# Kernel tuning notes

Hardware: AMD Instinct MI355X
Metric: run time of the kernel (lower is better)

Reference implementation:

```python
import jax, jax.numpy as jnp
import numpy as np

B, SQ, SKV, D = 16, 2048, 2048, 256

def setup_inputs() -> dict:
    key = jax.random.key(0)
    k1, k2, k3 = jax.random.split(key, 3)
    x = jax.random.normal(k1, (B, SQ, D), dtype=jnp.float32)
    y = jax.random.normal(k2, (B, SKV, D), dtype=jnp.float32)
    attn_mask = jax.random.normal(k3, (B, SQ, SKV), dtype=jnp.float32)
    dropout = 0  # p=0 -> deterministic (F.dropout with p=0 is identity)
    return {"x": x, "y": y, "attn_mask": attn_mask, "dropout": dropout}

def reference(x, y, attn_mask, dropout):
    # qk = x @ y^T : [B, Sq, Skv]
    qk = jnp.einsum('bqd,bkd->bqk', x, y)
    # NOTE: original scales mask by 1/sqrt(y.size(-2)) = 1/sqrt(Skv), not sqrt(D)
    scale_factor = attn_mask / (y.shape[-2] ** 0.5)
    scaled_qk = qk * scale_factor  # multiplicative per-element mask
    softmax_qk = jax.nn.softmax(scaled_qk, axis=-1)
    # dropout p=0 -> identity (deterministic baseline)
    dropout_qk = softmax_qk
    output = jnp.einsum('bqk,bkd->bqd', dropout_qk, y)
    return output + x
```

## Files before the change

kernel.cpp:

```cpp
#include <hip/hip_runtime.h>
#include <stdint.h>

typedef unsigned short u16;
typedef unsigned int   u32;

#define NB   16
#define SQL  2048
#define SKVL 2048
#define DHD  256
#define SCALE 0.022097086912079612f

typedef __bf16 bf16x8 __attribute__((ext_vector_type(8)));
typedef float  f32x4  __attribute__((ext_vector_type(4)));
typedef float  f32x16 __attribute__((ext_vector_type(16)));

__device__ __forceinline__ u16 f2b(float f) {
    union { float f; u32 i; } v; v.f = f;
    u32 x = v.i;
    return (u16)((x + 0x7fffu + ((x >> 16) & 1u)) >> 16);
}

__device__ __forceinline__ void async_cp16(const void* g, void* l) {
    __builtin_amdgcn_global_load_lds(
        (const __attribute__((address_space(1))) u32*)g,
        (__attribute__((address_space(3))) u32*)l, 16, 0, 0);
}

__global__ __launch_bounds__(256)
void prepass(const float* __restrict__ y, u16* __restrict__ ws)
{
    u16* yb  = ws;
    u16* ybT = ws + 8388608;

    const int tid = threadIdx.x;
    if (blockIdx.x < 512) {
        const int b   = blockIdx.x >> 5;
        const int seg = blockIdx.x & 31;
        const int r   = tid >> 2;
        const int dq  = tid & 3;
        const int kvg = seg * 64 + r;
        const float* src = y + ((size_t)(b * SKVL + kvg)) * DHD + dq * 64;
        u16* dst = yb + ((size_t)(b * SKVL + kvg)) * DHD;
        #pragma unroll
        for (int j = 0; j < 8; ++j) {
            const float4 a = *(const float4*)(src + j * 8);
            const float4 c4 = *(const float4*)(src + j * 8 + 4);
            union { u32 w[4]; uint4 q; } u;
            u.w[0] = (u32)f2b(a.x)  | ((u32)f2b(a.y)  << 16);
            u.w[1] = (u32)f2b(a.z)  | ((u32)f2b(a.w)  << 16);
            u.w[2] = (u32)f2b(c4.x) | ((u32)f2b(c4.y) << 16);
            u.w[3] = (u32)f2b(c4.z) | ((u32)f2b(c4.w) << 16);
            const int pos = (dq * 8 + j) ^ (kvg & 7);
            *(uint4*)(dst + pos * 8) = u.q;
        }
    } else {
        const int j     = blockIdx.x - 512;
        const int b     = j >> 5;
        const int kvblk = j & 31;
        const int d     = tid;
        const int kv0   = kvblk * 64;
        u16* dst = ybT + ((size_t)(b * 32 + kvblk)) * 16384 + d * 64;
        #pragma unroll
        for (int c = 0; c < 8; ++c) {
            float v[8];
            #pragma unroll
            for (int e = 0; e < 8; ++e)
                v[e] = y[((size_t)(b * SKVL + kv0 + 8 * c + e)) * DHD + d];
            union { u32 w[4]; uint4 q; } u;
            #pragma unroll
            for (int i = 0; i < 4; ++i)
                u.w[i] = (u32)f2b(v[2 * i]) | ((u32)f2b(v[2 * i + 1]) << 16);
            const int p = c ^ (d & 7);
            *(uint4*)(dst + p * 8) = u.q;
        }
    }
}

#define WAITBAR(str)                                          \
    do {                                                      \
        asm volatile("s_waitcnt " str ::: "memory");          \
        __builtin_amdgcn_sched_barrier(0);                    \
        __builtin_amdgcn_s_barrier();                         \
        __builtin_amdgcn_sched_barrier(0);                    \
    } while (0)

__global__ __launch_bounds__(256, 2)
void fa_main(const float* __restrict__ x, const float* __restrict__ mask,
             const u16* __restrict__ ws, float* __restrict__ out)
{
    __shared__ __align__(16) u16 Ks[16384];
    __shared__ __align__(16) u16 Vt[16384];
    __shared__ __align__(16) u16 Ps[64 * 72];
    __shared__ float Lred[2][64];

    const u16* yb  = ws;
    const u16* ybT = ws + 8388608;

    const int tid  = threadIdx.x;
    const int wv   = tid >> 6;
    const int lane = tid & 63;
    const int n    = lane & 31;
    const int hi   = lane >> 5;
    const int qh   = wv & 1;
    const int kh   = wv >> 1;

    const int b  = blockIdx.x >> 5;
    const int q0 = (blockIdx.x & 31) * 64;

    bf16x8 qfrag[16];
    {
        const float* xq = x + ((size_t)(b * SQL + q0 + 32 * qh + n)) * DHD + 8 * hi;
        #pragma unroll
        for (int s = 0; s < 16; ++s) {
            const float4 a  = *(const float4*)(xq + s * 16);
            const float4 c4 = *(const float4*)(xq + s * 16 + 4);
            union { u32 w[4]; bf16x8 v; } u;
            u.w[0] = (u32)f2b(a.x)  | ((u32)f2b(a.y)  << 16);
            u.w[1] = (u32)f2b(a.z)  | ((u32)f2b(a.w)  << 16);
            u.w[2] = (u32)f2b(c4.x) | ((u32)f2b(c4.y) << 16);
            u.w[3] = (u32)f2b(c4.z) | ((u32)f2b(c4.w) << 16);
            qfrag[s] = u.v;
        }
    }

    f32x16 o0 = {}, o1 = {}, o2 = {}, o3 = {};
    float lsum[16];
    #pragma unroll
    for (int r = 0; r < 16; ++r) lsum[r] = 0.f;

    const float* mrow = mask + ((size_t)(b * SQL + q0 + 32 * qh + 4 * hi)) * SKVL
                             + 32 * kh + n;
    #define ROFF(r) ((size_t)(((r) & 3) + 8 * ((r) >> 2)) * SKVL)

    float mkc[16], mkn[16];
    #pragma unroll
    for (int r = 0; r < 16; ++r) mkc[r] = mrow[ROFF(r)];

    {
        const char* gk = (const char*)(yb + ((size_t)b * SKVL) * DHD) + wv * 8192 + lane * 16;
        const char* gv = (const char*)(ybT + ((size_t)b * 32) * 16384) + wv * 8192 + lane * 16;
        char* lk = ((char*)Ks) + wv * 8192;
        char* lv = ((char*)Vt) + wv * 8192;
        #pragma unroll
        for (int i = 0; i < 8; ++i) { async_cp16(gk + i * 1024, lk + i * 1024);
                                      async_cp16(gv + i * 1024, lv + i * 1024); }
    }
    WAITBAR("vmcnt(0) lgkmcnt(0)");

    for (int it = 0; it < 32; ++it) {
        const size_t kvn = (it + 1 < 32) ? (size_t)(it + 1) * 64 : 0;
        #pragma unroll
        for (int r = 0; r < 16; ++r) mkn[r] = mrow[ROFF(r) + kvn];

        f32x16 sacc = {};
        const int kvloc = 32 * kh + n;
        __builtin_amdgcn_s_setprio(1);
        #pragma unroll
        for (int s = 0; s < 16; ++s) {
            const int p = (2 * s + hi) ^ (kvloc & 7);
            bf16x8 bf = *(const bf16x8*)(&Ks[kvloc * 256 + p * 8]);
            sacc = __builtin_amdgcn_mfma_f32_32x32x16_bf16(qfrag[s], bf, sacc, 0, 0, 0);
        }
        __builtin_amdgcn_s_setprio(0);

        #pragma unroll
        for (int r = 0; r < 16; ++r) {
            const int rowloc = (r & 3) + 8 * (r >> 2) + 4 * hi;
            float pv = __expf(sacc[r] * mkc[r] * SCALE);
            lsum[r] += pv;
            Ps[(32 * qh + rowloc) * 72 + 32 * kh + n] = f2b(pv);
        }

        WAITBAR("vmcnt(16) lgkmcnt(0)");

        if (it + 1 < 32) {
            const char* gk = (const char*)(yb + ((size_t)(b * SKVL + (it + 1) * 64)) * DHD)
                             + wv * 8192 + lane * 16;
            char* lk = ((char*)Ks) + wv * 8192;
            #pragma unroll
            for (int i = 0; i < 8; ++i) async_cp16(gk + i * 1024, lk + i * 1024);
        }

        bf16x8 pa[4];
        #pragma unroll
        for (int s = 0; s < 4; ++s)
            pa[s] = *(const bf16x8*)(&Ps[(32 * qh + n) * 72 + 16 * s + 8 * hi]);
        __builtin_amdgcn_s_setprio(1);
        #pragma unroll
        for (int t = 0; t < 4; ++t) {
            const int d = 128 * kh + 32 * t + n;
            f32x16 acc = (t == 0) ? o0 : (t == 1) ? o1 : (t == 2) ? o2 : o3;
            #pragma unroll
            for (int s = 0; s < 4; ++s) {
                const int p = (2 * s + hi) ^ (d & 7);
                bf16x8 bf = *(const bf16x8*)(&Vt[d * 64 + p * 8]);
                acc = __builtin_amdgcn_mfma_f32_32x32x16_bf16(pa[s], bf, acc, 0, 0, 0);
            }
            if (t == 0) o0 = acc; else if (t == 1) o1 = acc; else if (t == 2) o2 = acc; else o3 = acc;
        }
        __builtin_amdgcn_s_setprio(0);

        WAITBAR("lgkmcnt(0)");

        if (it + 1 < 32) {
            const char* gv = (const char*)(ybT + ((size_t)(b * 32 + it + 1)) * 16384)
                             + wv * 8192 + lane * 16;
            char* lv = ((char*)Vt) + wv * 8192;
            #pragma unroll
            for (int i = 0; i < 8; ++i) async_cp16(gv + i * 1024, lv + i * 1024);
        }

        WAITBAR("vmcnt(8) lgkmcnt(0)");

        #pragma unroll
        for (int r = 0; r < 16; ++r) mkc[r] = mkn[r];
    }

    #pragma unroll
    for (int r = 0; r < 16; ++r) {
        float v = lsum[r];
        v += __shfl_xor(v, 1);
        v += __shfl_xor(v, 2);
        v += __shfl_xor(v, 4);
        v += __shfl_xor(v, 8);
        v += __shfl_xor(v, 16);
        if (n == 0) {
            const int rowloc = (r & 3) + 8 * (r >> 2) + 4 * hi;
            Lred[kh][32 * qh + rowloc] = v;
        }
    }
    __syncthreads();

    float inv[16];
    #pragma unroll
    for (int r = 0; r < 16; ++r) {
        const int qloc = 32 * qh + (r & 3) + 8 * (r >> 2) + 4 * hi;
        inv[r] = 1.0f / (Lred[0][qloc] + Lred[1][qloc]);
    }

    #pragma unroll
    for (int r = 0; r < 16; ++r) {
        const int qloc = 32 * qh + (r & 3) + 8 * (r >> 2) + 4 * hi;
        const size_t rowoff = ((size_t)(b * SQL + q0 + qloc)) * DHD;
        #pragma unroll
        for (int t = 0; t < 4; ++t) {
            const int d = 128 * kh + 32 * t + n;
            const float ov = (t == 0) ? o0[r] : (t == 1) ? o1[r] : (t == 2) ? o2[r] : o3[r];
            out[rowoff + d] = ov * inv[r] + x[rowoff + d];
        }
    }
}

#define FKSS 264
#define FVTG 328
#define FPSS 40

__global__ __launch_bounds__(256, 2)
void fa_fallback(const float* __restrict__ x, const float* __restrict__ y,
                 const float* __restrict__ mask, float* __restrict__ out)
{
    __shared__ __align__(16) u16 Ks[32 * FKSS];
    __shared__ __align__(16) u32 Vt[16 * FVTG];
    __shared__ __align__(16) u16 Ps[64 * FPSS];

    const int tid  = threadIdx.x;
    const int wv   = tid >> 6;
    const int lane = tid & 63;
    const int l16  = lane & 15;
    const int quad = lane >> 4;
    const int b  = blockIdx.x >> 5;
    const int q0 = (blockIdx.x & 31) * 64;

    bf16x8 qfrag[8];
    {
        const float* xq = x + ((size_t)(b * SQL + q0 + wv * 16 + l16)) * DHD + quad * 8;
        #pragma unroll
        for (int s = 0; s < 8; ++s) {
            const float4 a = *(const float4*)(xq + s * 32);
            const float4 c = *(const float4*)(xq + s * 32 + 4);
            union { u32 w[4]; bf16x8 v; } u;
            u.w[0] = (u32)f2b(a.x) | ((u32)f2b(a.y) << 16);
            u.w[1] = (u32)f2b(a.z) | ((u32)f2b(a.w) << 16);
            u.w[2] = (u32)f2b(c.x) | ((u32)f2b(c.y) << 16);
            u.w[3] = (u32)f2b(c.z) | ((u32)f2b(c.w) << 16);
            qfrag[s] = u.v;
        }
    }
    f32x4 o[16] = {};
    float ls[4] = {0.f, 0.f, 0.f, 0.f};
    const int kv2 = tid & 15;
    const int dc  = tid >> 4;
    const float* ybase = y + ((size_t)b * SKVL) * DHD;
    float4 r0[4], r1[4];
    {
        const float* p0 = ybase + (size_t)(2 * kv2) * DHD + dc * 16;
        const float* p1 = p0 + DHD;
        #pragma unroll
        for (int p = 0; p < 4; ++p) { r0[p] = *(const float4*)(p0 + p * 4);
                                      r1[p] = *(const float4*)(p1 + p * 4); }
    }
    const float* mbase = mask + ((size_t)(b * SQL + q0 + wv * 16 + quad * 4)) * SKVL;
    float mkc0[4], mkc1[4], mkn0[4], mkn1[4];
    #pragma unroll
    for (int r = 0; r < 4; ++r) {
        const float* mp = mbase + (size_t)r * SKVL;
        mkc0[r] = mp[l16]; mkc1[r] = mp[16 + l16];
    }
    for (int it = 0; it < 64; ++it) {
        const int kv0 = it * 32;
        __syncthreads();
        {
            u16 e0[16], e1[16];
            #pragma unroll
            for (int p = 0; p < 4; ++p) {
                e0[p*4+0]=f2b(r0[p].x); e0[p*4+1]=f2b(r0[p].y);
                e0[p*4+2]=f2b(r0[p].z); e0[p*4+3]=f2b(r0[p].w);
                e1[p*4+0]=f2b(r1[p].x); e1[p*4+1]=f2b(r1[p].y);
                e1[p*4+2]=f2b(r1[p].z); e1[p*4+3]=f2b(r1[p].w);
            }
            union { u32 w[4]; uint4 q; } k0a, k0b, k1a, k1b;
            #pragma unroll
            for (int i = 0; i < 4; ++i) {
                k0a.w[i] = (u32)e0[2*i]   | ((u32)e0[2*i+1]   << 16);
                k0b.w[i] = (u32)e0[8+2*i] | ((u32)e0[8+2*i+1] << 16);
                k1a.w[i] = (u32)e1[2*i]   | ((u32)e1[2*i+1]   << 16);
                k1b.w[i] = (u32)e1[8+2*i] | ((u32)e1[8+2*i+1] << 16);
            }
            *(uint4*)(&Ks[(2*kv2)  *FKSS + dc*16])     = k0a.q;
            *(uint4*)(&Ks[(2*kv2)  *FKSS + dc*16 + 8]) = k0b.q;
            *(uint4*)(&Ks[(2*kv2+1)*FKSS + dc*16])     = k1a.q;
            *(uint4*)(&Ks[(2*kv2+1)*FKSS + dc*16 + 8]) = k1b.q;
            #pragma unroll
            for (int e = 0; e < 16; ++e)
                Vt[dc*FVTG + e*20 + kv2] = (u32)e0[e] | ((u32)e1[e] << 16);
        }
        __syncthreads();
        if (it + 1 < 64) {
            const float* p0 = ybase + (size_t)(kv0 + 32 + 2 * kv2) * DHD + dc * 16;
            const float* p1 = p0 + DHD;
            #pragma unroll
            for (int p = 0; p < 4; ++p) { r0[p] = *(const float4*)(p0 + p * 4);
                                          r1[p] = *(const float4*)(p1 + p * 4); }
        }
        {
            const int kvn2 = (it + 1 < 64) ? (kv0 + 32) : 0;
            #pragma unroll
            for (int r = 0; r < 4; ++r) {
                const float* mp = mbase + (size_t)r * SKVL + kvn2;
                mkn0[r] = mp[l16]; mkn1[r] = mp[16 + l16];
            }
        }
        f32x4 acc0 = {}, acc1 = {};
        #pragma unroll
        for (int s = 0; s < 8; ++s) {
            bf16x8 b0 = *(const bf16x8*)(&Ks[ l16     * FKSS + s*32 + quad*8]);
            bf16x8 b1 = *(const bf16x8*)(&Ks[(16+l16) * FKSS + s*32 + quad*8]);
            acc0 = __builtin_amdgcn_mfma_f32_16x16x32_bf16(qfrag[s], b0, acc0, 0, 0, 0);
            acc1 = __builtin_amdgcn_mfma_f32_16x16x32_bf16(qfrag[s], b1, acc1, 0, 0, 0);
        }
        #pragma unroll
        for (int r = 0; r < 4; ++r) {
            float p0 = __expf(acc0[r] * mkc0[r] * SCALE);
            float p1 = __expf(acc1[r] * mkc1[r] * SCALE);
            ls[r] += p0 + p1;
            u16* pr = &Ps[(wv*16 + quad*4 + r) * FPSS];
            pr[l16]      = f2b(p0);
            pr[16 + l16] = f2b(p1);
        }
        bf16x8 afrag = *(const bf16x8*)(&Ps[(wv*16 + l16) * FPSS + quad*8]);
        #pragma unroll
        for (int t = 0; t < 16; ++t) {
            bf16x8 bfrag = *(const bf16x8*)(&Vt[t*FVTG + l16*20 + quad*4]);
            o[t] = __builtin_amdgcn_mfma_f32_16x16x32_bf16(afrag, bfrag, o[t], 0, 0, 0);
        }
        #pragma unroll
        for (int r = 0; r < 4; ++r) { mkc0[r] = mkn0[r]; mkc1[r] = mkn1[r]; }
    }
    #pragma unroll
    for (int r = 0; r < 4; ++r) {
        float v = ls[r];
        v += __shfl_xor(v, 1); v += __shfl_xor(v, 2);
        v += __shfl_xor(v, 4); v += __shfl_xor(v, 8);
        ls[r] = 1.0f / v;
    }
    const int qrow = q0 + wv * 16 + quad * 4;
    #pragma unroll
    for (int r = 0; r < 4; ++r) {
        const size_t rowoff = ((size_t)(b * SQL + qrow + r)) * DHD;
        #pragma unroll
        for (int t = 0; t < 16; ++t) {
            const int d = t * 16 + l16;
            out[rowoff + d] = o[t][r] * ls[r] + x[rowoff + d];
        }
    }
}

extern "C" void kernel_launch(void* const* d_in, const int* in_sizes, int n_in,
                              void* d_out, int out_size, void* d_ws, size_t ws_size,
                              hipStream_t stream) {
    const float* x    = (const float*)d_in[0];
    const float* y    = (const float*)d_in[1];
    const float* mask = (const float*)d_in[2];
    float* out        = (float*)d_out;

    if (ws_size >= 33554432ull) {
        prepass<<<1024, 256, 0, stream>>>(y, (u16*)d_ws);
        fa_main<<<512, 256, 0, stream>>>(x, mask, (const u16*)d_ws, out);
    } else {
        fa_fallback<<<512, 256, 0, stream>>>(x, y, mask, out);
    }
}
```

Before: 469.8 us.

## Load V fragments directly from global in MFMA layout and double-buffer K in LDS

The prepass now writes V in a per-lane MFMA fragment layout, so each wave loads its V operand straight from global memory into registers and never stages it through LDS. The LDS space freed by dropping the V buffer becomes a second K buffer, giving K double-buffering with a single barrier pair per iteration instead of three. The K swizzle widens from 8 to 32 slots, and the mask prefetch moves to after the softmax. In exchange, each iteration now waits for all outstanding memory loads at its end, and the V register arrays raise register pressure.

```diff
diff --git a/kernel.cpp b/kernel.cpp
--- a/kernel.cpp
+++ b/kernel.cpp
@@ -30,7 +30,7 @@
 void prepass(const float* __restrict__ y, u16* __restrict__ ws)
 {
     u16* yb  = ws;
-    u16* ybT = ws + 8388608;
+    u16* ybF = ws + 8388608;
 
     const int tid = threadIdx.x;
     if (blockIdx.x < 512) {
@@ -50,18 +50,21 @@
             u.w[1] = (u32)f2b(a.z)  | ((u32)f2b(a.w)  << 16);
             u.w[2] = (u32)f2b(c4.x) | ((u32)f2b(c4.y) << 16);
             u.w[3] = (u32)f2b(c4.z) | ((u32)f2b(c4.w) << 16);
-            const int pos = (dq * 8 + j) ^ (kvg & 7);
+            const int pos = (dq * 8 + j) ^ (kvg & 31);
             *(uint4*)(dst + pos * 8) = u.q;
         }
     } else {
         const int j     = blockIdx.x - 512;
         const int b     = j >> 5;
-        const int kvblk = j & 31;
+        const int it    = j & 31;
         const int d     = tid;
-        const int kv0   = kvblk * 64;
-        u16* dst = ybT + ((size_t)(b * 32 + kvblk)) * 16384 + d * 64;
+        const int kv0   = it * 64;
+        const int kh = d >> 7, t = (d >> 5) & 3, n = d & 31;
+        u16* dst = ybF + ((size_t)(b * 32 + it)) * 16384 + kh * 8192 + t * 2048 + n * 8;
         #pragma unroll
         for (int c = 0; c < 8; ++c) {
+            const int s  = c >> 1;
+            const int hi = c & 1;
             float v[8];
             #pragma unroll
             for (int e = 0; e < 8; ++e)
@@ -70,8 +73,7 @@
             #pragma unroll
             for (int i = 0; i < 4; ++i)
                 u.w[i] = (u32)f2b(v[2 * i]) | ((u32)f2b(v[2 * i + 1]) << 16);
-            const int p = c ^ (d & 7);
-            *(uint4*)(dst + p * 8) = u.q;
+            *(uint4*)(dst + s * 512 + hi * 256) = u.q;
         }
     }
 }
@@ -88,13 +90,12 @@
 void fa_main(const float* __restrict__ x, const float* __restrict__ mask,
              const u16* __restrict__ ws, float* __restrict__ out)
 {
-    __shared__ __align__(16) u16 Ks[16384];
-    __shared__ __align__(16) u16 Vt[16384];
+    __shared__ __align__(16) u16 Ks[2][16384];
     __shared__ __align__(16) u16 Ps[64 * 72];
     __shared__ float Lred[2][64];
 
     const u16* yb  = ws;
-    const u16* ybT = ws + 8388608;
+    const u16* ybF = ws + 8388608;
 
     const int tid  = threadIdx.x;
     const int wv   = tid >> 6;
@@ -132,33 +133,44 @@
                              + 32 * kh + n;
     #define ROFF(r) ((size_t)(((r) & 3) + 8 * ((r) >> 2)) * SKVL)
 
-    float mkc[16], mkn[16];
-    #pragma unroll
-    for (int r = 0; r < 16; ++r) mkc[r] = mrow[ROFF(r)];
+    float mk[16];
+    #pragma unroll
+    for (int r = 0; r < 16; ++r) mk[r] = mrow[ROFF(r)];
+
+    const u16* vfb = ybF + ((size_t)(b * 32)) * 16384 + kh * 8192 + lane * 8;
 
     {
         const char* gk = (const char*)(yb + ((size_t)b * SKVL) * DHD) + wv * 8192 + lane * 16;
-        const char* gv = (const char*)(ybT + ((size_t)b * 32) * 16384) + wv * 8192 + lane * 16;
-        char* lk = ((char*)Ks) + wv * 8192;
-        char* lv = ((char*)Vt) + wv * 8192;
-        #pragma unroll
-        for (int i = 0; i < 8; ++i) { async_cp16(gk + i * 1024, lk + i * 1024);
-                                      async_cp16(gv + i * 1024, lv + i * 1024); }
+        char* lk = ((char*)&Ks[0][0]) + wv * 8192;
+        #pragma unroll
+        for (int i = 0; i < 8; ++i) async_cp16(gk + i * 1024, lk + i * 1024);
     }
     WAITBAR("vmcnt(0) lgkmcnt(0)");
 
     for (int it = 0; it < 32; ++it) {
-        const size_t kvn = (it + 1 < 32) ? (size_t)(it + 1) * 64 : 0;
-        #pragma unroll
-        for (int r = 0; r < 16; ++r) mkn[r] = mrow[ROFF(r) + kvn];
+        const u16* kbuf = &Ks[it & 1][0];
+
+        if (it + 1 < 32) {
+            const char* gk = (const char*)(yb + ((size_t)(b * SKVL + (it + 1) * 64)) * DHD)
+                             + wv * 8192 + lane * 16;
+            char* lk = ((char*)&Ks[(it + 1) & 1][0]) + wv * 8192;
+            #pragma unroll
+            for (int i = 0; i < 8; ++i) async_cp16(gk + i * 1024, lk + i * 1024);
+        }
+
+        const u16* vft = vfb + (size_t)it * 16384;
+        bf16x8 va[8];
+        #pragma unroll
+        for (int f = 0; f < 8; ++f)
+            va[f] = *(const bf16x8*)(vft + f * 512);
 
         f32x16 sacc = {};
         const int kvloc = 32 * kh + n;
         __builtin_amdgcn_s_setprio(1);
         #pragma unroll
         for (int s = 0; s < 16; ++s) {
-            const int p = (2 * s + hi) ^ (kvloc & 7);
-            bf16x8 bf = *(const bf16x8*)(&Ks[kvloc * 256 + p * 8]);
+            const int p = (2 * s + hi) ^ (kvloc & 31);
+            bf16x8 bf = *(const bf16x8*)(&kbuf[kvloc * 256 + p * 8]);
             sacc = __builtin_amdgcn_mfma_f32_32x32x16_bf16(qfrag[s], bf, sacc, 0, 0, 0);
         }
         __builtin_amdgcn_s_setprio(0);
@@ -166,19 +178,22 @@
         #pragma unroll
         for (int r = 0; r < 16; ++r) {
             const int rowloc = (r & 3) + 8 * (r >> 2) + 4 * hi;
-            float pv = __expf(sacc[r] * mkc[r] * SCALE);
+            float pv = __expf(sacc[r] * mk[r] * SCALE);
             lsum[r] += pv;
             Ps[(32 * qh + rowloc) * 72 + 32 * kh + n] = f2b(pv);
         }
 
-        WAITBAR("vmcnt(16) lgkmcnt(0)");
+        WAITBAR("lgkmcnt(0)");
+
+        bf16x8 vb[8];
+        #pragma unroll
+        for (int f = 0; f < 8; ++f)
+            vb[f] = *(const bf16x8*)(vft + 4096 + f * 512);
 
         if (it + 1 < 32) {
-            const char* gk = (const char*)(yb + ((size_t)(b * SKVL + (it + 1) * 64)) * DHD)
-                             + wv * 8192 + lane * 16;
-            char* lk = ((char*)Ks) + wv * 8192;
-            #pragma unroll
-            for (int i = 0; i < 8; ++i) async_cp16(gk + i * 1024, lk + i * 1024);
+            const size_t kvn = (size_t)(it + 1) * 64;
+            #pragma unroll
+            for (int r = 0; r < 16; ++r) mk[r] = mrow[ROFF(r) + kvn];
         }
 
         bf16x8 pa[4];
@@ -188,32 +203,17 @@
         __builtin_amdgcn_s_setprio(1);
         #pragma unroll
         for (int t = 0; t < 4; ++t) {
-            const int d = 128 * kh + 32 * t + n;
             f32x16 acc = (t == 0) ? o0 : (t == 1) ? o1 : (t == 2) ? o2 : o3;
             #pragma unroll
             for (int s = 0; s < 4; ++s) {
-                const int p = (2 * s + hi) ^ (d & 7);
-                bf16x8 bf = *(const bf16x8*)(&Vt[d * 64 + p * 8]);
+                bf16x8 bf = (t < 2) ? va[t * 4 + s] : vb[(t - 2) * 4 + s];
                 acc = __builtin_amdgcn_mfma_f32_32x32x16_bf16(pa[s], bf, acc, 0, 0, 0);
             }
             if (t == 0) o0 = acc; else if (t == 1) o1 = acc; else if (t == 2) o2 = acc; else o3 = acc;
         }
         __builtin_amdgcn_s_setprio(0);
 
-        WAITBAR("lgkmcnt(0)");
-
-        if (it + 1 < 32) {
-            const char* gv = (const char*)(ybT + ((size_t)(b * 32 + it + 1)) * 16384)
-                             + wv * 8192 + lane * 16;
-            char* lv = ((char*)Vt) + wv * 8192;
-            #pragma unroll
-            for (int i = 0; i < 8; ++i) async_cp16(gv + i * 1024, lv + i * 1024);
-        }
-
-        WAITBAR("vmcnt(8) lgkmcnt(0)");
-
-        #pragma unroll
-        for (int r = 0; r < 16; ++r) mkc[r] = mkn[r];
+        WAITBAR("vmcnt(0) lgkmcnt(0)");
     }
 
     #pragma unroll
```

New measurement: 521.9 us. 1.11x slower.
